# Optimization experiments

Measured on AMD Instinct MI355X. Metric: run time of the kernel, lower is better.

Reference implementation:

```python
import jax, jax.numpy as jnp
import numpy as np

N_STATES = 16
HIDDEN = 100   # HIDDEN1_SIZE in the original
SEQ_LEN = 250000


def setup_inputs() -> dict:
    key = jax.random.key(0)
    k1, k2, k3 = jax.random.split(key, 3)
    rx = jax.random.normal(k1, (SEQ_LEN, 1), dtype=jnp.float32)
    # net parameters, torch Linear layout: W [out, in], b [out]
    W1 = jax.random.normal(k2, (HIDDEN, 1), dtype=jnp.float32) * 1.0          # fan_in = 1
    b1 = jnp.zeros((HIDDEN,), dtype=jnp.float32)
    W2 = jax.random.normal(k3, (N_STATES, HIDDEN), dtype=jnp.float32) * 0.1   # ~1/sqrt(100)
    b2 = jnp.zeros((N_STATES,), dtype=jnp.float32)
    return {"rx": rx, "W1": W1, "b1": b1, "W2": W2, "b2": b2}


def reference(rx, W1, b1, W2, b2):
    """VNETDetector.forward with phase=Phase.TEST.

    Returns (detected_word [T,1], confident_bits [T,1], confidence_word [T,1]).
    """
    n_states = W2.shape[0]
    # create_transition_table: row i = previous states [2i mod n, (2i+1) mod n]
    trans = (2 * jnp.arange(n_states)[:, None] + jnp.arange(2)[None, :]) % n_states  # [n_states, 2]

    # priors = log(softmax(net(rx)))  (detached in original; forward math identical)
    h = jax.nn.relu(rx @ W1.T + b1)             # [T, HIDDEN]
    logits = h @ W2.T + b2                      # [T, n_states]
    log_probs = jax.nn.log_softmax(logits, axis=1)
    probs = jnp.exp(log_probs)

    confident_bits = (jnp.argmax(probs, axis=1) % 2).reshape(-1, 1)      # int
    confidence_word = jnp.max(probs, axis=1).reshape(-1, 1)

    # Viterbi-like add-compare-select trellis, sequential over time -> lax.scan
    llrs = -log_probs  # [T, n_states]

    def acs_step(in_prob, llr):
        # detected bit BEFORE updating the path metrics (matches original loop order)
        bit = jnp.argmin(in_prob) % 2
        path = in_prob + llr                    # [n_states]
        out_prob = jnp.min(path[trans], axis=1) # compare-select over the 2 incoming edges
        return out_prob, bit

    in_prob0 = jnp.zeros((n_states,), dtype=rx.dtype)
    _, bits = jax.lax.scan(acs_step, in_prob0, llrs)
    detected_word = bits.astype(rx.dtype).reshape(-1, 1)  # [T, 1], broadcast like torch row assign

    return detected_word, confident_bits, confidence_word
```

## Files before the change

### kernel.cpp

```cpp
#include <hip/hip_runtime.h>
#include <math.h>


#define T_LEN 250000
#define HID   100
#define NTIL  1954

typedef const __attribute__((address_space(1))) void* gas_t;
typedef __attribute__((address_space(3)))       void* las_t;

static __device__ float4 g_llr2[NTIL * 512];
static __device__ float4 g_state2[NTIL * 2048];
static __device__ float  g_sink[256];
static __device__ int    g_flag;
static __device__ int    g_isf32;

__global__ void VNETDetector_3942779978170_kernel() {}

__device__ __forceinline__ float ld_in(const void* p, long i, int f32) {
    if (f32) return ((const float*)p)[i];
    unsigned w = (unsigned)((const unsigned short*)p)[i] << 16;
    return __uint_as_float(w);
}
__device__ __forceinline__ void st_out(void* p, long i, float v, int f32) {
    if (f32) { ((float*)p)[i] = v; return; }
    unsigned u = __float_as_uint(v);
    ((unsigned short*)p)[i] = (unsigned short)((u + 0x7FFFu + ((u >> 16) & 1u)) >> 16);
}

template<int CTRL>
__device__ __forceinline__ float dppf(float x) {
    return __int_as_float(__builtin_amdgcn_mov_dpp(
        __float_as_int(x), CTRL, 0xF, 0xF, true));
}

__global__ void k0_detect(const unsigned short* __restrict__ w1u) {
    if (threadIdx.x != 0) return;
    int outliers = 0;
    for (int k = 0; k < 64; k++) {
        int e = (w1u[k] >> 7) & 0xFF;
        outliers += (e < 100 || e > 140) ? 1 : 0;
    }
    g_isf32 = (outliers >= 8) ? 1 : 0;
}

__global__ __launch_bounds__(256) void k1_mlp(
        const void* __restrict__ rx, const void* __restrict__ W1,
        const void* __restrict__ b1, const void* __restrict__ W2,
        const void* __restrict__ b2, void* __restrict__ out)
{
    __shared__ float w1s[HID], b1s[HID], w2s[HID * 16], b2s[16];
    int f32 = g_isf32;
    for (int i = threadIdx.x; i < HID; i += 256) {
        w1s[i] = ld_in(W1, i, f32);
        b1s[i] = ld_in(b1, i, f32);
    }
    for (int i = threadIdx.x; i < HID * 16; i += 256) {
        int j = i >> 4, s = i & 15;
        w2s[i] = ld_in(W2, s * HID + j, f32);
    }
    if (threadIdx.x < 16) b2s[threadIdx.x] = ld_in(b2, threadIdx.x, f32);
    __syncthreads();

    int t = blockIdx.x * 256 + threadIdx.x;
    if (t >= T_LEN) return;
    float x = ld_in(rx, t, f32);

    float acc[16];
#pragma unroll
    for (int s = 0; s < 16; s++) acc[s] = 0.0f;
    for (int j = 0; j < HID; j++) {
        float h = __fmul_rn(x, w1s[j]);
        h = __fadd_rn(h, b1s[j]);
        h = h > 0.0f ? h : 0.0f;
        const float* w = &w2s[j * 16];
#pragma unroll
        for (int s = 0; s < 16; s++) acc[s] = fmaf(h, w[s], acc[s]);
    }
    float logits[16];
#pragma unroll
    for (int s = 0; s < 16; s++) logits[s] = __fadd_rn(acc[s], b2s[s]);

    float m = logits[0];
#pragma unroll
    for (int s = 1; s < 16; s++) m = fmaxf(m, logits[s]);
    float y[16], e[16];
#pragma unroll
    for (int s = 0; s < 16; s++) {
        y[s] = __fsub_rn(logits[s], m);
        e[s] = (float)exp((double)y[s]);
    }
    float r[8];
#pragma unroll
    for (int j = 0; j < 8; j++) r[j] = __fadd_rn(e[j], e[j + 8]);
    float s01 = __fadd_rn(r[0], r[1]), s23 = __fadd_rn(r[2], r[3]);
    float s45 = __fadd_rn(r[4], r[5]), s67 = __fadd_rn(r[6], r[7]);
    float S = __fadd_rn(__fadd_rn(s01, s23), __fadd_rn(s45, s67));
    float logS = (float)log((double)S);

    int grp = t >> 2, sub = t & 3;
    float* l2 = (float*)g_llr2 + (long)grp * 64 + sub;
    float p[16];
#pragma unroll
    for (int s = 0; s < 16; s++) {
        float lp = __fsub_rn(y[s], logS);
        int e0 = s & 1, e1 = (s >> 1) & 1, e2 = (s >> 2) & 1, e3 = (s >> 3) & 1;
        int jj;
        if      (sub == 0) jj = (e0^e2) | ((e1^e2)<<1) | (e2<<2) | (e3<<3);
        else if (sub == 1) jj = (e1^e3) | ((e0^e1)<<1) | (e1<<2) | (e2<<3);
        else if (sub == 2) jj = (e0^e2) | ((e0^e3)<<1) | (e0<<2) | (e1<<3);
        else               jj = (e1^e3) | ((e2^e3)<<1) | (e3<<2) | (e0<<3);
        l2[jj * 4] = -lp;
        p[s] = (float)exp((double)lp);
    }
    float best = p[0]; int bi = 0;
#pragma unroll
    for (int s = 1; s < 16; s++)
        if (p[s] > best) { best = p[s]; bi = s; }
    st_out(out, (long)T_LEN + t, (float)(bi & 1), f32);
    st_out(out, 2L * T_LEN + t,  best,           f32);
}

#define STEP4(Q, ST, GOFF)                                                    \
    {                                                                         \
        float4 sv;                                                            \
        sv.x = V;                                                             \
        { float P = __fadd_rn(V, (Q).x);                                      \
          V = fminf(dppf<0xB1>(P), P); }                        \
        sv.y = V;                                                             \
        { float P = __fadd_rn(V, (Q).y);                                      \
          V = fminf(dppf<0x4E>(P), P); }                        \
        sv.z = V;                                                             \
        { float P = __fadd_rn(V, (Q).z);                                      \
          V = fminf(dppf<0x141>(P), P); }                       \
        sv.w = V;                                                             \
        (ST)[GOFF] = sv;                                                      \
        { float P = __fadd_rn(V, (Q).w);                                      \
          V = fminf(dppf<0x128>(P), P); }                       \
    }

__device__ __forceinline__ void stage8(const float4* g, float4* lbuf, int lane) {
#pragma unroll
    for (int k = 0; k < 8; k++)
        __builtin_amdgcn_global_load_lds((gas_t)(g + k * 64 + lane),
                                         (las_t)(lbuf + k * 64), 16, 0, 0);
}

#define PRIME(BUF)                                                            \
    { _Pragma("unroll")                                                       \
      for (int r = 0; r < 8; r++) ring[r] = (BUF)[r * 16 + jj]; }

#define PHASE(BUF, TI)                                                        \
    {                                                                         \
        float4* st = g_state2 + (long)(TI) * 2048 + j;  \
        _Pragma("unroll")                                                     \
        for (int gg = 0; gg < 32; gg++) {                                     \
            float4 q = ring[gg & 7];                                          \
            if (gg < 24) ring[gg & 7] = (BUF)[(gg + 8) * 16 + jj];            \
            STEP4(q, st, gg * 64)                                             \
        }                                                                     \
    }

__global__ __launch_bounds__(64) void k2_scan()
{
    __shared__ float4 ldsA[512];
    __shared__ float4 ldsB[512];

    if (blockIdx.x != 0) {
        float a = (float)(threadIdx.x + 1) * 1e-8f;
        float b = 1.0000001f, c = 0.9999999f;
        int phase = 0, idle = 0;
        for (long i = 0; i < 3500000; i++) {
#pragma unroll
            for (int u = 0; u < 8; u++) a = fmaf(a, b, c);
            if ((i & 127) == 0) {
                int f = __hip_atomic_load(&g_flag, __ATOMIC_RELAXED,
                                          __HIP_MEMORY_SCOPE_AGENT);
                if (phase == 0) {
                    if (f) phase = 1;
                    else if (++idle > 512) break;
                } else if (!f) break;
            }
        }
        g_sink[blockIdx.x] = a;
        return;
    }

    int j  = threadIdx.x;
    if (j == 0)
        __hip_atomic_store(&g_flag, 1, __ATOMIC_RELAXED, __HIP_MEMORY_SCOPE_AGENT);
    int jj = j & 15;

    float V = 0.0f;
    float4 ring[8];

    stage8(g_llr2, ldsA, j);
    asm volatile("s_waitcnt vmcnt(0)" ::: "memory");
    PRIME(ldsA)

    for (int t2 = 0; t2 < NTIL; t2 += 2) {
        stage8(g_llr2 + (long)(t2 + 1) * 512, ldsB, j);
        PHASE(ldsA, t2)
        asm volatile("s_waitcnt vmcnt(32)" ::: "memory");
        PRIME(ldsB)
        if (t2 + 2 < NTIL) stage8(g_llr2 + (long)(t2 + 2) * 512, ldsA, j);
        PHASE(ldsB, t2 + 1)
        asm volatile("s_waitcnt vmcnt(32)" ::: "memory");
        if (t2 + 2 < NTIL) PRIME(ldsA)
    }

    if (j == 0)
        __hip_atomic_store(&g_flag, 0, __ATOMIC_RELAXED, __HIP_MEMORY_SCOPE_AGENT);
}

__global__ __launch_bounds__(256) void k3_bits(void* __restrict__ out)
{
    int t = blockIdx.x * 256 + threadIdx.x;
    if (t >= T_LEN) return;
    int grp = t >> 2, s = t & 3;
    const float4* base = g_state2 + (long)grp * 64;
    float v[8];
#pragma unroll
    for (int k = 0; k < 8; k++) {
        int k0 = k & 1, k1 = (k >> 1) & 1, k2v = (k >> 2) & 1;
        int jk;
        if      (s == 0) jk = (k0^k2v) | ((k1^k2v)<<1) | (k2v<<2);
        else if (s == 1) jk = ((k0^k1)<<1) | (k1<<2) | (k2v<<3);
        else if (s == 2) jk = (k0^k2v) | (k0<<2) | (k1<<3);
        else             jk = k1 | (k2v<<1) | (k0<<3);
        v[k] = ((const float*)(base + jk))[s];
    }
    float best = v[0]; int idx = 0;
#pragma unroll
    for (int k = 1; k < 8; k++)
        if (v[k] < best) { best = v[k]; idx = k; }
    st_out(out, t, (float)(idx & 1), g_isf32);
}

extern "C" void kernel_launch(void* const* d_in, const int* in_sizes, int n_in,
                              void* d_out, int out_size, void* d_ws, size_t ws_size,
                              hipStream_t stream)
{
    const void* rx = d_in[0];
    const void* W1 = d_in[1];
    const void* b1 = d_in[2];
    const void* W2 = d_in[3];
    const void* b2 = d_in[4];

    k0_detect<<<1,   64,  0, stream>>>((const unsigned short*)W1);
    k1_mlp   <<<977, 256, 0, stream>>>(rx, W1, b1, W2, b2, d_out);
    k2_scan  <<<256, 64,  0, stream>>>();
    k3_bits  <<<977, 256, 0, stream>>>(d_out);
}
```

Before: 3.540 ms.

## Checkpoint scan state every 16 steps and recompute bits in parallel pass

The serial scan now stores path metrics only once every 16 time steps instead of every step, which cuts its global store traffic about 16x and relaxes the vmcnt wait. The MLP kernel also writes the LLRs in natural layout. The bits kernel then replays the add-compare-select for 16 steps per thread from each checkpoint to recover every argmin bit. This moves store pressure off the sequential critical path, at the cost of extra LLR writes and a small parallel recompute.

```diff
diff --git a/kernel.cpp b/kernel.cpp
--- a/kernel.cpp
+++ b/kernel.cpp
@@ -5,12 +5,14 @@
 #define T_LEN 250000
 #define HID   100
 #define NTIL  1954
+#define NSEG  15625
 
 typedef const __attribute__((address_space(1))) void* gas_t;
 typedef __attribute__((address_space(3)))       void* las_t;
 
 static __device__ float4 g_llr2[NTIL * 512];
-static __device__ float4 g_state2[NTIL * 2048];
+static __device__ float  g_llrN[T_LEN * 16];
+static __device__ float  g_state3[NTIL * 8 * 64];
 static __device__ float  g_sink[256];
 static __device__ int    g_flag;
 static __device__ int    g_isf32;
@@ -100,19 +102,27 @@
 
     int grp = t >> 2, sub = t & 3;
     float* l2 = (float*)g_llr2 + (long)grp * 64 + sub;
+    float ln[16];
     float p[16];
 #pragma unroll
     for (int s = 0; s < 16; s++) {
         float lp = __fsub_rn(y[s], logS);
+        float llr = -lp;
+        ln[s] = llr;
         int e0 = s & 1, e1 = (s >> 1) & 1, e2 = (s >> 2) & 1, e3 = (s >> 3) & 1;
         int jj;
         if      (sub == 0) jj = (e0^e2) | ((e1^e2)<<1) | (e2<<2) | (e3<<3);
         else if (sub == 1) jj = (e1^e3) | ((e0^e1)<<1) | (e1<<2) | (e2<<3);
         else if (sub == 2) jj = (e0^e2) | ((e0^e3)<<1) | (e0<<2) | (e1<<3);
         else               jj = (e1^e3) | ((e2^e3)<<1) | (e3<<2) | (e0<<3);
-        l2[jj * 4] = -lp;
+        l2[jj * 4] = llr;
         p[s] = (float)exp((double)lp);
     }
+    float4* ln4 = (float4*)(g_llrN + (long)t * 16);
+#pragma unroll
+    for (int q4 = 0; q4 < 4; q4++)
+        ln4[q4] = (float4){ln[q4*4], ln[q4*4+1], ln[q4*4+2], ln[q4*4+3]};
+
     float best = p[0]; int bi = 0;
 #pragma unroll
     for (int s = 1; s < 16; s++)
@@ -121,20 +131,14 @@
     st_out(out, 2L * T_LEN + t,  best,           f32);
 }
 
-#define STEP4(Q, ST, GOFF)                                                    \
+#define STEP4(Q)                                                              \
     {                                                                         \
-        float4 sv;                                                            \
-        sv.x = V;                                                             \
         { float P = __fadd_rn(V, (Q).x);                                      \
           V = fminf(dppf<0xB1>(P), P); }                        \
-        sv.y = V;                                                             \
         { float P = __fadd_rn(V, (Q).y);                                      \
           V = fminf(dppf<0x4E>(P), P); }                        \
-        sv.z = V;                                                             \
         { float P = __fadd_rn(V, (Q).z);                                      \
           V = fminf(dppf<0x141>(P), P); }                       \
-        sv.w = V;                                                             \
-        (ST)[GOFF] = sv;                                                      \
         { float P = __fadd_rn(V, (Q).w);                                      \
           V = fminf(dppf<0x128>(P), P); }                       \
     }
@@ -152,12 +156,13 @@
 
 #define PHASE(BUF, TI)                                                        \
     {                                                                         \
-        float4* st = g_state2 + (long)(TI) * 2048 + j;  \
+        float* st3 = g_state3 + (long)(TI) * 512 + j;       \
         _Pragma("unroll")                                                     \
         for (int gg = 0; gg < 32; gg++) {                                     \
+            if ((gg & 3) == 0) st3[(gg >> 2) * 64] = V;  \
             float4 q = ring[gg & 7];                                          \
             if (gg < 24) ring[gg & 7] = (BUF)[(gg + 8) * 16 + jj];            \
-            STEP4(q, st, gg * 64)                                             \
+            STEP4(q)                                                          \
         }                                                                     \
     }
 
@@ -201,11 +206,11 @@
     for (int t2 = 0; t2 < NTIL; t2 += 2) {
         stage8(g_llr2 + (long)(t2 + 1) * 512, ldsB, j);
         PHASE(ldsA, t2)
-        asm volatile("s_waitcnt vmcnt(32)" ::: "memory");
+        asm volatile("s_waitcnt vmcnt(8)" ::: "memory");
         PRIME(ldsB)
         if (t2 + 2 < NTIL) stage8(g_llr2 + (long)(t2 + 2) * 512, ldsA, j);
         PHASE(ldsB, t2 + 1)
-        asm volatile("s_waitcnt vmcnt(32)" ::: "memory");
+        asm volatile("s_waitcnt vmcnt(8)" ::: "memory");
         if (t2 + 2 < NTIL) PRIME(ldsA)
     }
 
@@ -215,26 +220,33 @@
 
 __global__ __launch_bounds__(256) void k3_bits(void* __restrict__ out)
 {
-    int t = blockIdx.x * 256 + threadIdx.x;
-    if (t >= T_LEN) return;
-    int grp = t >> 2, s = t & 3;
-    const float4* base = g_state2 + (long)grp * 64;
+    int seg = blockIdx.x * 256 + threadIdx.x;
+    if (seg >= NSEG) return;
+    int f32 = g_isf32;
+    const float* base = g_state3 + (long)seg * 64;
     float v[8];
 #pragma unroll
     for (int k = 0; k < 8; k++) {
         int k0 = k & 1, k1 = (k >> 1) & 1, k2v = (k >> 2) & 1;
-        int jk;
-        if      (s == 0) jk = (k0^k2v) | ((k1^k2v)<<1) | (k2v<<2);
-        else if (s == 1) jk = ((k0^k1)<<1) | (k1<<2) | (k2v<<3);
-        else if (s == 2) jk = (k0^k2v) | (k0<<2) | (k1<<3);
-        else             jk = k1 | (k2v<<1) | (k0<<3);
-        v[k] = ((const float*)(base + jk))[s];
-    }
-    float best = v[0]; int idx = 0;
-#pragma unroll
-    for (int k = 1; k < 8; k++)
-        if (v[k] < best) { best = v[k]; idx = k; }
-    st_out(out, t, (float)(idx & 1), g_isf32);
+        int jk = (k0^k2v) | ((k1^k2v) << 1) | (k2v << 2);
+        v[k] = base[jk];
+    }
+    const float* l = g_llrN + (long)seg * 256;
+#pragma unroll
+    for (int u = 0; u < 16; u++) {
+        float best = v[0]; int idx = 0;
+#pragma unroll
+        for (int k = 1; k < 8; k++)
+            if (v[k] < best) { best = v[k]; idx = k; }
+        st_out(out, (long)seg * 16 + u, (float)(idx & 1), f32);
+        float nv[8];
+#pragma unroll
+        for (int k = 0; k < 8; k++)
+            nv[k] = fminf(__fadd_rn(v[(2 * k) & 7],     l[u * 16 + 2 * k]),
+                          __fadd_rn(v[(2 * k + 1) & 7], l[u * 16 + 2 * k + 1]));
+#pragma unroll
+        for (int k = 0; k < 8; k++) v[k] = nv[k];
+    }
 }
 
 extern "C" void kernel_launch(void* const* d_in, const int* in_sizes, int n_in,
@@ -250,5 +262,5 @@
     k0_detect<<<1,   64,  0, stream>>>((const unsigned short*)W1);
     k1_mlp   <<<977, 256, 0, stream>>>(rx, W1, b1, W2, b2, d_out);
     k2_scan  <<<256, 64,  0, stream>>>();
-    k3_bits  <<<977, 256, 0, stream>>>(d_out);
-}
+    k3_bits  <<<62,  256, 0, stream>>>(d_out);
+}
```

After: 2.988 ms. 1.18x faster.
